# Performance work log

Hardware: AMD Instinct MI355X
Metric: run time of the kernel (lower is better)

Reference implementation:

```python
import jax, jax.numpy as jnp
import numpy as np

B, C, H, W = 64, 3, 512, 512
WEIGHT = 1.0


def _high_freq_mask(h, w):
    m = np.ones((h, w), dtype=np.float32)
    ch, cw = h // 2, w // 2
    m[ch - h // 8:ch + h // 8, cw - w // 8:cw + w // 8] = 0.0
    return jnp.asarray(m), float(m.sum())


def setup_inputs() -> dict:
    key = jax.random.key(0)
    k1, k2 = jax.random.split(key)
    # images in [-1, 1]
    generated = jax.random.uniform(k1, (B, C, H, W), dtype=jnp.float32, minval=-1.0, maxval=1.0)
    target = jax.random.uniform(k2, (B, C, H, W), dtype=jnp.float32, minval=-1.0, maxval=1.0)
    return {"generated": generated, "target": target}


def _to_gray01(x):
    # (B,3,H,W) in [-1,1] -> (B,H,W) grayscale in [0,1]
    g = x[:, 0] * 0.299 + x[:, 1] * 0.587 + x[:, 2] * 0.114
    return (g + 1.0) * 0.5


def _high_freq_psd(gray):
    # gray: (B,H,W) float32
    h, w = gray.shape[-2:]
    mask, count = _high_freq_mask(h, w)
    fft = jnp.fft.fftshift(jnp.fft.fft2(gray), axes=(-2, -1))  # (B,H,W) complex64
    psd = jnp.real(fft) ** 2 + jnp.imag(fft) ** 2
    psd_log = jnp.log10(psd + 1e-10)
    # mean over high-frequency (masked) region; count is static
    return jnp.sum(psd_log * mask, axis=(-2, -1)) / count  # (B,)


def reference(generated, target):
    psd_gen = _high_freq_psd(_to_gray01(generated))
    psd_tgt = _high_freq_psd(_to_gray01(target))
    loss = jnp.mean(jnp.abs(psd_gen - psd_tgt))  # F.l1_loss
    return WEIGHT * loss
```

## Files before the change

### kernel.cpp

```cpp
#include <hip/hip_runtime.h>
#include <math.h>

#ifndef M_PI
#define M_PI 3.14159265358979323846
#endif


__device__ __forceinline__ float2 cmulf(float2 a, float2 b) {
    return make_float2(fmaf(a.x, b.x, -(a.y * b.y)), fmaf(a.x, b.y, a.y * b.x));
}
__device__ __forceinline__ float2 caddf(float2 a, float2 b){ return make_float2(a.x+b.x, a.y+b.y); }
__device__ __forceinline__ float2 csubf(float2 a, float2 b){ return make_float2(a.x-b.x, a.y-b.y); }

__device__ __forceinline__ void lds_order() {
    __builtin_amdgcn_sched_barrier(0);
}

__device__ __forceinline__ void dft8(float2 v[8]) {
    const float S = 0.70710678118654752440f;
    float2 a0=caddf(v[0],v[4]), a1=caddf(v[1],v[5]), a2=caddf(v[2],v[6]), a3=caddf(v[3],v[7]);
    float2 b0=csubf(v[0],v[4]);
    float2 t1=csubf(v[1],v[5]);
    float2 t2=csubf(v[2],v[6]);
    float2 t3=csubf(v[3],v[7]);
    float2 b1=make_float2(S*(t1.x+t1.y), S*(t1.y-t1.x));
    float2 b2=make_float2(t2.y, -t2.x);
    float2 b3=make_float2(S*(t3.y-t3.x), -S*(t3.x+t3.y));
    float2 c0=caddf(a0,a2), c1=caddf(a1,a3), c2=csubf(a0,a2);
    float2 u3=csubf(a1,a3); float2 c3=make_float2(u3.y,-u3.x);
    float2 d0=caddf(b0,b2), d1=caddf(b1,b3), d2=csubf(b0,b2);
    float2 w3=csubf(b1,b3); float2 d3=make_float2(w3.y,-w3.x);
    v[0]=caddf(c0,c1); v[4]=csubf(c0,c1);
    v[2]=caddf(c2,c3); v[6]=csubf(c2,c3);
    v[1]=caddf(d0,d1); v[5]=csubf(d0,d1);
    v[3]=caddf(d2,d3); v[7]=csubf(d2,d3);
}

__device__ __forceinline__ void twapply(float2 v[8], float2 w) {
    const float2 w2 = cmulf(w,  w);
    const float2 w3 = cmulf(w2, w);
    const float2 w4 = cmulf(w2, w2);
    const float2 w5 = cmulf(w2, w3);
    const float2 w6 = cmulf(w3, w3);
    const float2 w7 = cmulf(w4, w3);
    v[1] = cmulf(v[1], w);
    v[2] = cmulf(v[2], w2);
    v[3] = cmulf(v[3], w3);
    v[4] = cmulf(v[4], w4);
    v[5] = cmulf(v[5], w5);
    v[6] = cmulf(v[6], w6);
    v[7] = cmulf(v[7], w7);
}

__device__ __forceinline__ void fft512_reg(float2 v[8], float2* __restrict__ W,
                                           const float2* __restrict__ twg, int lane) {
    dft8(v);
    twapply(v, twg[lane]);
#pragma unroll
    for (int c = 0; c < 8; ++c) W[(c<<6) + ((lane + 2*c)&63)] = v[c];
    lds_order();
    {
        const int c = lane>>3, p = lane&7, base = c<<6, off = p + 2*c;
#pragma unroll
        for (int bb = 0; bb < 8; ++bb) v[bb] = W[base + (((bb<<3) + off)&63)];
    }
    lds_order();
    dft8(v);
    twapply(v, twg[(lane&7)<<3]);
    {
        const int c = lane>>3, p = lane&7, base = c<<6, r2 = 2*c;
#pragma unroll
        for (int d = 0; d < 8; ++d) W[base + (((d<<3) + (p^d) + r2)&63)] = v[d];
    }
    lds_order();
    {
        const int c = lane>>3, d = lane&7, base = c<<6, off = (d<<3) + 2*c;
#pragma unroll
        for (int p = 0; p < 8; ++p) v[p] = W[base + ((off + (p^d))&63)];
    }
    lds_order();
    dft8(v);
}

__global__ void twiddle_kernel(float2* __restrict__ tw) {
    const int k = threadIdx.x;
    const double ang = -2.0 * M_PI * (double)k / 512.0;
    tw[k] = make_float2((float)cos(ang), (float)sin(ang));
}

__global__ __launch_bounds__(512, 4)
void row_fft_kernel(const float* __restrict__ gen, const float* __restrict__ tgt,
                    const float2* __restrict__ twg, float2* __restrict__ scratch,
                    int b0) {
    __shared__ float2 SBUF[8 * 512];
    const int tid = threadIdx.x, wave = tid>>6, lane = tid&63;
    const int img = blockIdx.x>>6, rg = blockIdx.x&63;
    const int b = b0 + img, r = (rg<<3) + wave;

    const size_t rowoff = ((size_t)b * 3 * 512 + r) * 512;
    const float* gR = gen + rowoff; const float* gG = gR + 262144; const float* gB = gG + 262144;
    const float* tR = tgt + rowoff; const float* tG = tR + 262144; const float* tB = tG + 262144;

    float2 v[8];
#pragma unroll
    for (int a = 0; a < 8; ++a) {
        const int idx = (a<<6) + lane;
        const float gg = fmaf(0.299f, gR[idx], fmaf(0.587f, gG[idx], fmaf(0.114f, gB[idx], 1.0f))) * 0.5f;
        const float tt = fmaf(0.299f, tR[idx], fmaf(0.587f, tG[idx], fmaf(0.114f, tB[idx], 1.0f))) * 0.5f;
        v[a] = make_float2(gg, tt);
    }

    float2* W = SBUF + (wave<<9);
    fft512_reg(v, W, twg, lane);

#pragma unroll
    for (int e = 0; e < 8; ++e) {
        const int col = (e<<6) + lane;
        W[(col + (wave<<3)) & 511] = v[e];
    }
    __syncthreads();

    const size_t obase = ((size_t)img << 18) + ((size_t)rg << 12);
    const int colr = tid>>3, j = tid&7;
    float2* sj = SBUF + (j<<9);
#pragma unroll
    for (int it = 0; it < 8; ++it) {
        const int col = colr + (it<<6);
        scratch[obase + (it<<9) + tid] = sj[(col + (j<<3)) & 511];
    }
}

__device__ __forceinline__ void accum_psd(float2 F1, float2 F2, double& sg, double& st) {
    const float ar = 0.5f*(F1.x + F2.x), ai = 0.5f*(F1.y - F2.y);
    const float br = 0.5f*(F1.y + F2.y), bi = 0.5f*(F2.x - F1.x);
    const float pg = fmaf(ar, ar, ai*ai) + 1e-10f;
    const float pt = fmaf(br, br, bi*bi) + 1e-10f;
    sg += (double)log10f(pg);
    st += (double)log10f(pt);
}

__global__ __launch_bounds__(256, 4)
void col_fft_reduce_kernel(const float2* __restrict__ scratch,
                           const float2* __restrict__ twg,
                           double2* __restrict__ partial, int b0) {
    __shared__ float2 SBUF[4 * 512];
    const int tid = threadIdx.x, wave = tid>>6, lane = tid&63;
    const int gw = (blockIdx.x<<2) + wave;
    const int img = gw>>8, t = gw&255;
    const int b = b0 + img;
    const int kxA = t;
    const int kxB = (t == 0) ? 256 : 512 - t;
    const int colA = ((kxA>>6)<<6) + ((kxA&7)<<3) + ((kxA>>3)&7);
    const int colB = ((kxB>>6)<<6) + ((kxB&7)<<3) + ((kxB>>3)&7);
    float2* W = SBUF + (wave<<9);

    const size_t lanoff = ((size_t)(lane>>3)<<12) + (lane&7);
    const float2* srcA = scratch + ((size_t)img<<18) + ((size_t)colA<<3) + lanoff;
    const float2* srcB = scratch + ((size_t)img<<18) + ((size_t)colB<<3) + lanoff;
    float2 va[8], vb[8];
#pragma unroll
    for (int a = 0; a < 8; ++a) va[a] = srcA[a<<15];
#pragma unroll
    for (int a = 0; a < 8; ++a) vb[a] = srcB[a<<15];

    fft512_reg(va, W, twg, lane);

    const int cc = lane>>3, dd = lane&7;
    const int kyb = cc + (dd<<3);

#pragma unroll
    for (int e = 0; e < 8; ++e) W[kyb + (e<<6)] = va[e];
    lds_order();
    float2 aRev[8];
#pragma unroll
    for (int e = 0; e < 8; ++e) aRev[e] = W[(512 - (kyb + (e<<6))) & 511];
    lds_order();

    fft512_reg(vb, W, twg, lane);

#pragma unroll
    for (int e = 0; e < 8; ++e) W[kyb + (e<<6)] = vb[e];
    lds_order();
    float2 bRev[8];
#pragma unroll
    for (int e = 0; e < 8; ++e) bRev[e] = W[(512 - (kyb + (e<<6))) & 511];
    lds_order();

    const bool kxinA = (t < 64);
    const bool kxinB = (t >= 1 && t <= 64);

    double sg = 0.0, st = 0.0;
    if (t == 0) {
#pragma unroll
        for (int e = 0; e < 8; ++e) {
            if (!(kxinA && (e == 0 || e == 7))) accum_psd(va[e], aRev[e], sg, st);
            accum_psd(vb[e], bRev[e], sg, st);
        }
    } else {
#pragma unroll
        for (int e = 0; e < 8; ++e) {
            if (!(kxinA && (e == 0 || e == 7))) accum_psd(va[e], bRev[e], sg, st);
            if (!(kxinB && (e == 0 || e == 7))) accum_psd(vb[e], aRev[e], sg, st);
        }
    }
#pragma unroll
    for (int off = 32; off; off >>= 1) {
        sg += __shfl_down(sg, off);
        st += __shfl_down(st, off);
    }
    if (lane == 0) partial[((size_t)b<<8) + t] = make_double2(sg, st);
}

__global__ __launch_bounds__(256)
void reduce_partial_kernel(const double2* __restrict__ partial,
                           double* __restrict__ accum) {
    __shared__ double2 red[4];
    const int img = blockIdx.x, tid = threadIdx.x, wave = tid>>6, lane = tid&63;
    const double2 p = partial[((size_t)img<<8) + tid];
    double sg = p.x, st = p.y;
#pragma unroll
    for (int off = 32; off; off >>= 1) {
        sg += __shfl_down(sg, off);
        st += __shfl_down(st, off);
    }
    if (lane == 0) red[wave] = make_double2(sg, st);
    __syncthreads();
    if (tid == 0) {
        double SG = 0.0, ST = 0.0;
#pragma unroll
        for (int w = 0; w < 4; ++w) { SG += red[w].x; ST += red[w].y; }
        accum[img] = SG;
        accum[64 + img] = ST;
    }
}

__global__ void finalize_kernel(const double* __restrict__ accum,
                                float* __restrict__ out) {
    const int lane = threadIdx.x;
    double d = fabs(accum[lane] - accum[64 + lane]) * (1.0 / 245760.0);
#pragma unroll
    for (int off = 32; off; off >>= 1) d += __shfl_down(d, off);
    if (lane == 0) out[0] = (float)(d * (1.0 / 64.0));
}

extern "C" void kernel_launch(void* const* d_in, const int* in_sizes, int n_in,
                              void* d_out, int out_size, void* d_ws, size_t ws_size,
                              hipStream_t stream) {
    (void)in_sizes; (void)n_in; (void)out_size;
    const float* gen = (const float*)d_in[0];
    const float* tgt = (const float*)d_in[1];
    float*   out     = (float*)d_out;
    float2*  tw      = (float2*)d_ws;
    double*  accum   = (double*)((char*)d_ws + 2048);
    double2* partial = (double2*)((char*)d_ws + 4096);
    float2*  scratch = (float2*)((char*)d_ws + 266240);

    const size_t per_img = (size_t)512 * 512 * sizeof(float2);
    const size_t avail = (ws_size > 266240) ? (ws_size - 266240) : 0;
    int chunk = 64;
    while (chunk > 1 && (size_t)chunk * per_img > avail) chunk >>= 1;

    twiddle_kernel<<<1, 256, 0, stream>>>(tw);
    for (int b0 = 0; b0 < 64; b0 += chunk) {
        row_fft_kernel<<<dim3(chunk * 64), dim3(512), 0, stream>>>(gen, tgt, tw, scratch, b0);
        col_fft_reduce_kernel<<<dim3(chunk * 64), dim3(256), 0, stream>>>(scratch, tw, partial, b0);
    }
    reduce_partial_kernel<<<dim3(64), dim3(256), 0, stream>>>(partial, accum);
    finalize_kernel<<<1, 64, 0, stream>>>(accum, out);
}
```

Before: 492.7 us.

## Shrink row-FFT blocks to 4 rows, retile scratch layout, add XCD block swizzle

Row FFT blocks now handle 4 rows with 256 threads instead of 8 rows with 512, so the transposed scratch tiles are 4-row groups and the column kernel's gather indexing is changed to match. Both kernels also remap block IDs with an XCD swizzle so that neighbouring logical blocks land on the same chiplet, aiming for better L2 locality. The smaller blocks should raise occupancy, but the column kernel now reads 4-element contiguous runs instead of 8, which may make its global loads less coalesced.

New measurement: 506.8 us. 2.9% more time.

```diff
diff --git a/kernel.cpp b/kernel.cpp
--- a/kernel.cpp
+++ b/kernel.cpp
@@ -11,6 +11,10 @@
 }
 __device__ __forceinline__ float2 caddf(float2 a, float2 b){ return make_float2(a.x+b.x, a.y+b.y); }
 __device__ __forceinline__ float2 csubf(float2 a, float2 b){ return make_float2(a.x-b.x, a.y-b.y); }
+
+__device__ __forceinline__ int xcd_swizzle(int b, int nwg) {
+    return (b & 7) * (nwg >> 3) + (b >> 3);
+}
 
 __device__ __forceinline__ void lds_order() {
     __builtin_amdgcn_sched_barrier(0);
@@ -88,14 +92,15 @@
     tw[k] = make_float2((float)cos(ang), (float)sin(ang));
 }
 
-__global__ __launch_bounds__(512, 4)
+__global__ __launch_bounds__(256, 8)
 void row_fft_kernel(const float* __restrict__ gen, const float* __restrict__ tgt,
                     const float2* __restrict__ twg, float2* __restrict__ scratch,
-                    int b0) {
-    __shared__ float2 SBUF[8 * 512];
+                    int b0, int nwg) {
+    __shared__ float2 SBUF[4 * 512];
+    const int w = xcd_swizzle((int)blockIdx.x, nwg);
     const int tid = threadIdx.x, wave = tid>>6, lane = tid&63;
-    const int img = blockIdx.x>>6, rg = blockIdx.x&63;
-    const int b = b0 + img, r = (rg<<3) + wave;
+    const int img = w>>7, rg4 = w&127;
+    const int b = b0 + img, r = (rg4<<2) + wave;
 
     const size_t rowoff = ((size_t)b * 3 * 512 + r) * 512;
     const float* gR = gen + rowoff; const float* gG = gR + 262144; const float* gB = gG + 262144;
@@ -120,13 +125,13 @@
     }
     __syncthreads();
 
-    const size_t obase = ((size_t)img << 18) + ((size_t)rg << 12);
-    const int colr = tid>>3, j = tid&7;
-    float2* sj = SBUF + (j<<9);
+    const size_t obase = ((size_t)img << 18) + ((size_t)rg4 << 11);
+    const int cg = tid>>2, j4 = tid&3;
+    float2* sj = SBUF + (j4<<9);
 #pragma unroll
     for (int it = 0; it < 8; ++it) {
-        const int col = colr + (it<<6);
-        scratch[obase + (it<<9) + tid] = sj[(col + (j<<3)) & 511];
+        const int col = cg + (it<<6);
+        scratch[obase + (it<<8) + tid] = sj[(col + (j4<<3)) & 511];
     }
 }
 
@@ -142,10 +147,11 @@
 __global__ __launch_bounds__(256, 4)
 void col_fft_reduce_kernel(const float2* __restrict__ scratch,
                            const float2* __restrict__ twg,
-                           double2* __restrict__ partial, int b0) {
+                           double2* __restrict__ partial, int b0, int nwg) {
     __shared__ float2 SBUF[4 * 512];
+    const int w = xcd_swizzle((int)blockIdx.x, nwg);
     const int tid = threadIdx.x, wave = tid>>6, lane = tid&63;
-    const int gw = (blockIdx.x<<2) + wave;
+    const int gw = (w<<2) + wave;
     const int img = gw>>8, t = gw&255;
     const int b = b0 + img;
     const int kxA = t;
@@ -154,9 +160,9 @@
     const int colB = ((kxB>>6)<<6) + ((kxB&7)<<3) + ((kxB>>3)&7);
     float2* W = SBUF + (wave<<9);
 
-    const size_t lanoff = ((size_t)(lane>>3)<<12) + (lane&7);
-    const float2* srcA = scratch + ((size_t)img<<18) + ((size_t)colA<<3) + lanoff;
-    const float2* srcB = scratch + ((size_t)img<<18) + ((size_t)colB<<3) + lanoff;
+    const size_t lanoff = ((size_t)(lane>>2)<<11) + (lane&3);
+    const float2* srcA = scratch + ((size_t)img<<18) + ((size_t)colA<<2) + lanoff;
+    const float2* srcB = scratch + ((size_t)img<<18) + ((size_t)colB<<2) + lanoff;
     float2 va[8], vb[8];
 #pragma unroll
     for (int a = 0; a < 8; ++a) va[a] = srcA[a<<15];
@@ -262,8 +268,10 @@
 
     twiddle_kernel<<<1, 256, 0, stream>>>(tw);
     for (int b0 = 0; b0 < 64; b0 += chunk) {
-        row_fft_kernel<<<dim3(chunk * 64), dim3(512), 0, stream>>>(gen, tgt, tw, scratch, b0);
-        col_fft_reduce_kernel<<<dim3(chunk * 64), dim3(256), 0, stream>>>(scratch, tw, partial, b0);
+        const int nwr = chunk * 128;
+        const int nwc = chunk * 64;
+        row_fft_kernel<<<dim3(nwr), dim3(256), 0, stream>>>(gen, tgt, tw, scratch, b0, nwr);
+        col_fft_reduce_kernel<<<dim3(nwc), dim3(256), 0, stream>>>(scratch, tw, partial, b0, nwc);
     }
     reduce_partial_kernel<<<dim3(64), dim3(256), 0, stream>>>(partial, accum);
     finalize_kernel<<<1, 64, 0, stream>>>(accum, out);
```
